# Optimization experiments

Measured on AMD Instinct MI355X. Metric: run time of the kernel, lower is better.

## Reference

```python
import jax, jax.numpy as jnp
import numpy as np

NU, B, N, D = 3, 16, 1024, 256  # n_utils, batch, tokens per util, embed dim


def l2norm(x, axis=-1, eps=1e-12):
    # F.normalize over channel dim: x / max(||x||_2, eps)
    n = jnp.linalg.norm(x, axis=axis, keepdims=True)
    return x / jnp.maximum(n, eps)


def setup_inputs() -> dict:
    key = jax.random.key(0)
    ks = jax.random.split(key, 20)
    s = 0.05
    return {
        "u0": jax.random.normal(ks[0], (B, N, D), jnp.float32),
        "u1": jax.random.normal(ks[1], (B, N, D), jnp.float32),
        "u2": jax.random.normal(ks[2], (B, N, D), jnp.float32),
        # Unary per util: embed Conv1d(D,D,1), feature_reduce Conv1d(D,1,1)
        "Wu": jax.random.normal(ks[3], (NU, D, D), jnp.float32) * s,
        "bu": jax.random.normal(ks[4], (NU, D), jnp.float32) * s,
        "wr": jax.random.normal(ks[5], (NU, D), jnp.float32) * s,
        "br": jax.random.normal(ks[6], (NU,), jnp.float32) * s,
        # Self Pairwise per util: embed_X, embed_Y Conv1d(D,D,1)
        "Wsx": jax.random.normal(ks[7], (NU, D, D), jnp.float32) * s,
        "bsx": jax.random.normal(ks[8], (NU, D), jnp.float32) * s,
        "Wsy": jax.random.normal(ks[9], (NU, D, D), jnp.float32) * s,
        "bsy": jax.random.normal(ks[10], (NU, D), jnp.float32) * s,
        # Cross Pairwise per ordered pair (i,j), i!=j (diagonal unused)
        "Wpx": jax.random.normal(ks[11], (NU, NU, D, D), jnp.float32) * s,
        "bpx": jax.random.normal(ks[12], (NU, NU, D), jnp.float32) * s,
        "Wpy": jax.random.normal(ks[13], (NU, NU, D, D), jnp.float32) * s,
        "bpy": jax.random.normal(ks[14], (NU, NU, D), jnp.float32) * s,
        # reduce_potentials: (i,i) -> Conv1d(4,1,1,bias=False); (i,j) -> Conv1d(3,1,1,bias=False)
        "wdiag": jax.random.normal(ks[15], (NU, 4), jnp.float32) * s,
        "wpair": jax.random.normal(ks[16], (NU, NU, 3), jnp.float32) * s,
    }


def _forward(u0, u1, u2, Wu, bu, wr, br, Wsx, bsx, Wsy, bsy,
             Wpx, bpx, Wpy, bpy, wdiag, wpair):
    U = jnp.stack([u0, u1, u2])  # (NU, b, n, d)

    # --- Unary potentials (eval mode: dropout = identity) ---
    Xe = jnp.einsum('ubnd,ued->ubne', U, Wu) + bu[:, None, None, :]
    unary = jnp.einsum('ubne,ue->ubn', jax.nn.relu(Xe), wr) + br[:, None, None]  # (NU,b,n)

    # --- Self Pairwise (x_spatial_dim=None path): embed, cosine-normalize over channels, affinity, mean ---
    Xs = l2norm(jnp.einsum('ubnd,ued->ubne', U, Wsx) + bsx[:, None, None, :])
    Ys = l2norm(jnp.einsum('ubnd,ued->ubne', U, Wsy) + bsy[:, None, None, :])
    S_self = jnp.einsum('ubne,ubme->ubnm', Xs, Ys)  # (NU,b,n,n)
    self_pot = S_self.mean(axis=3)                   # X_poten only (Y is None)  (NU,b,n)

    # --- Cross Pairwise over all ordered pairs (u,v) ---
    Xp = l2norm(jnp.einsum('ubnd,uved->uvbne', U, Wpx) + bpx[:, :, None, None, :])
    Yp = l2norm(jnp.einsum('vbnd,uved->uvbne', U, Wpy) + bpy[:, :, None, None, :])
    S = jnp.einsum('uvbne,uvbme->uvbnm', Xp, Yp)     # (NU,NU,b,n,n)
    pot_x = S.mean(axis=4)  # poten for util u in pair (u,v): (NU,NU,b,n)
    pot_y = S.mean(axis=3)  # poten for util v in pair (u,v): (NU,NU,b,n)

    # --- Reduce potentials per (target i, source j), softmax-attend over source tokens ---
    rows = []
    for i in range(NU):
        row = []
        for j in range(NU):
            if i == j:
                pots = [unary[i], self_pot[i]] + [pot_x[i, k] for k in range(NU) if k != i]
                w = wdiag[i]            # (4,)
            else:
                pots = [unary[j], self_pot[j], pot_y[i, j]]
                w = wpair[i, j]         # (3,)
            P = jnp.stack(pots, axis=1)                 # (b, k, n)
            red = jnp.einsum('bkn,k->bn', P, w)         # Conv1d(k,1,1,bias=False)
            a = jax.nn.softmax(red, axis=1)             # (b, n)
            row.append(jnp.einsum('bnd,bn->bd', U[j], a))  # attended feature (b, d)
        rows.append(jnp.stack(row))
    return jnp.stack(rows)  # (NU, NU, b, d)


def reference(u0, u1, u2, Wu, bu, wr, br, Wsx, bsx, Wsy, bsy,
              Wpx, bpx, Wpy, bpy, wdiag, wpair):
    return _forward(u0, u1, u2, Wu, bu, wr, br, Wsx, bsx, Wsy, bsy,
                    Wpx, bpx, Wpy, bpy, wdiag, wpair)
```

## Files before the change

kernel.cpp:

```cpp
#include <hip/hip_runtime.h>
#include <math.h>

#define NU 3
#define BB 16
#define NN 1024
#define DD 256
#define MM (BB*NN)
#define NPAIR 6

#define OFF_UNARY  0
#define OFF_INVXS  (OFF_UNARY + NU*MM)
#define OFF_INVXP  (OFF_INVXS + NU*MM)
#define OFF_INVYP  (OFF_INVXP + NPAIR*MM)
#define OFF_YBAR   (OFF_INVYP + NPAIR*MM)
#define OFF_XPBAR  (OFF_YBAR + NU*BB*DD)
#define OFF_YPBAR  (OFF_XPBAR + NPAIR*BB*DD)
#define OFF_PROJS  (OFF_YPBAR + NPAIR*BB*DD)
#define OFF_PROJX  (OFF_PROJS + NU*BB*DD)
#define OFF_PROJY  (OFF_PROJX + NPAIR*BB*DD)
#define OFF_CSS    (OFF_PROJY + NPAIR*BB*DD)
#define OFF_CSX    (OFF_CSS + NU*BB)
#define OFF_CSY    (OFF_CSX + NPAIR*BB)
#define OFF_SELFP  (OFF_CSY + NPAIR*BB)
#define OFF_POTX   (OFF_SELFP + NU*MM)
#define OFF_POTY   (OFF_POTX + NPAIR*MM)
#define WS_FLOATS  (OFF_POTY + NPAIR*MM)
#define OFF_PROB   (WS_FLOATS + 21*32768)
#define OFF_PART   (OFF_PROB + 9*BB*NN)

typedef _Float16 half8 __attribute__((ext_vector_type(8)));
typedef float f32x4 __attribute__((ext_vector_type(4)));

__device__ __forceinline__ const float* selU(int u, const float* u0, const float* u1, const float* u2) {
    return u == 0 ? u0 : (u == 1 ? u1 : u2);
}
__device__ __forceinline__ half8 cvt8(float4 a, float4 b) {
    half8 h = { (_Float16)a.x,(_Float16)a.y,(_Float16)a.z,(_Float16)a.w,
                (_Float16)b.x,(_Float16)b.y,(_Float16)b.z,(_Float16)b.w };
    return h;
}
__device__ __forceinline__ void gload16(const _Float16* g, _Float16* l) {
    __builtin_amdgcn_global_load_lds(
        (const __attribute__((address_space(1))) void*)g,
        (__attribute__((address_space(3))) void*)l,
        16, 0, 0);
}

__global__ __launch_bounds__(256) void convw_kernel(
    const float* __restrict__ Wu, const float* __restrict__ Wsx, const float* __restrict__ Wsy,
    const float* __restrict__ Wpx, const float* __restrict__ Wpy, float* __restrict__ ws)
{
    const int slot = blockIdx.x;
    const int kc   = blockIdx.y;
    const int tid  = threadIdx.x;
    const int u = slot / 7, s = slot % 7;
    const int j0 = (u==0)?1:0, j1 = (u==2)?1:2;
    const float* W =
        s==0 ? Wu  + (size_t)u*DD*DD :
        s==1 ? Wsx + (size_t)u*DD*DD :
        s==2 ? Wsy + (size_t)u*DD*DD :
        s==3 ? Wpx + (size_t)(u*NU+j0)*DD*DD :
        s==4 ? Wpx + (size_t)(u*NU+j1)*DD*DD :
        s==5 ? Wpy + (size_t)(j0*NU+u)*DD*DD :
               Wpy + (size_t)(j1*NU+u)*DD*DD;
    _Float16* wh = (_Float16*)(ws + WS_FLOATS) + (size_t)slot*65536 + (size_t)kc*8192;
    #pragma unroll
    for (int g = 0; g < 4; ++g) {
        const int idx16 = g*256 + tid;
        const int lane = idx16 & 63;
        const int e  = (idx16 >> 6)*16 + (lane & 15);
        const int k0 = kc*32 + (lane >> 4)*8;
        const float* sp = W + (size_t)e*DD + k0;
        const float4 v0 = *reinterpret_cast<const float4*>(sp);
        const float4 v1 = *reinterpret_cast<const float4*>(sp + 4);
        *reinterpret_cast<half8*>(wh + (size_t)idx16*8) = cvt8(v0, v1);
    }
}

__global__ __launch_bounds__(256, 2) void pass1_kernel(
    const float* __restrict__ u0, const float* __restrict__ u1, const float* __restrict__ u2,
    const float* __restrict__ bu, const float* __restrict__ wr, const float* __restrict__ br,
    const float* __restrict__ bsx, const float* __restrict__ bsy,
    const float* __restrict__ bpx, const float* __restrict__ bpy,
    float* __restrict__ ws)
{
    __shared__ __align__(16) _Float16 Ub[16384];
    __shared__ __align__(16) _Float16 Wb[2][8192];
    __shared__ float ep_sum[4][64];
    __shared__ float ep_inv[64];

    const int tid  = threadIdx.x;
    const int u    = blockIdx.y;
    const int row0 = blockIdx.x * 64;
    const int b    = row0 >> 10;

    const int j0 = (u==0)?1:0, j1 = (u==2)?1:2;
    const int px0 = u*2, px1 = u*2+1;
    const int py0 = (u==0)?2:((u==1)?0:1);
    const int py1 = (u==0)?4:((u==1)?5:3);

    const float* src = selU(u,u0,u1,u2);
    const _Float16* whU = (const _Float16*)(ws + WS_FLOATS) + (size_t)u*7*65536;

    const int lane = tid & 63, wq = tid >> 6;
    const int l15 = lane & 15, lg = lane >> 4;
    const int swz = (l15 >> 1) & 3;
    const int kxor = (lg ^ swz) * 8;

    f32x4 acc[4][4];
    #pragma unroll
    for (int m = 0; m < 4; ++m)
        #pragma unroll
        for (int n = 0; n < 4; ++n) acc[m][n] = (f32x4)0.f;

#define STAGE(T, BUF) { \
    const _Float16* gsb = whU + (size_t)((T) >> 3)*65536 + (size_t)((T) & 7)*8192 \
                        + (size_t)(wq*4)*512 + (size_t)lane*8; \
    _Pragma("unroll") \
    for (int i_ = 0; i_ < 4; ++i_) \
        gload16(gsb + i_*512, &Wb[BUF][(wq*4 + i_)*512]); }

    STAGE(0, 0)

    #pragma unroll
    for (int c = 0; c < 8; ++c) {
        const int G2 = c*256 + tid;
        const int t  = G2 >> 5;
        const int gk = G2 & 31;
        const int kc = gk >> 2, kg = gk & 3;
        const float* p = src + (size_t)(row0 + t)*DD + gk*8;
        const float4 v0 = *reinterpret_cast<const float4*>(p);
        const float4 v1 = *reinterpret_cast<const float4*>(p + 4);
        const int kgs = kg ^ ((t >> 1) & 3);
        *reinterpret_cast<half8*>(&Ub[kc*2048 + t*32 + kgs*8]) = cvt8(v0, v1);
    }
    __syncthreads();

    for (int s = 0; s < 7; ++s) {
        #pragma unroll
        for (int kc = 0; kc < 8; ++kc) {
            const int t = s*8 + kc;
            const int cur = t & 1;
            if (t < 55) STAGE(t+1, cur^1)
            half8 af0 = *reinterpret_cast<const half8*>(&Ub[kc*2048 + (     l15)*32 + kxor]);
            half8 af1 = *reinterpret_cast<const half8*>(&Ub[kc*2048 + (16 + l15)*32 + kxor]);
            half8 af2 = *reinterpret_cast<const half8*>(&Ub[kc*2048 + (32 + l15)*32 + kxor]);
            half8 af3 = *reinterpret_cast<const half8*>(&Ub[kc*2048 + (48 + l15)*32 + kxor]);
            #pragma unroll
            for (int n = 0; n < 4; ++n) {
                const half8 bf = *reinterpret_cast<const half8*>(&Wb[cur][(wq*4 + n)*512 + lane*8]);
                acc[0][n] = __builtin_amdgcn_mfma_f32_16x16x32_f16(af0, bf, acc[0][n],0,0,0);
                acc[1][n] = __builtin_amdgcn_mfma_f32_16x16x32_f16(af1, bf, acc[1][n],0,0,0);
                acc[2][n] = __builtin_amdgcn_mfma_f32_16x16x32_f16(af2, bf, acc[2][n],0,0,0);
                acc[3][n] = __builtin_amdgcn_mfma_f32_16x16x32_f16(af3, bf, acc[3][n],0,0,0);
            }
            __syncthreads();
        }

        const float* bias =
            s==0 ? bu  + u*DD :
            s==1 ? bsx + u*DD :
            s==2 ? bsy + u*DD :
            s==3 ? bpx + (u*NU+j0)*DD :
            s==4 ? bpx + (u*NU+j1)*DD :
            s==5 ? bpy + (j0*NU+u)*DD :
                   bpy + (j1*NU+u)*DD;
        float bv[4];
        #pragma unroll
        for (int n = 0; n < 4; ++n) bv[n] = bias[wq*64 + n*16 + l15];
        #pragma unroll
        for (int m = 0; m < 4; ++m)
            #pragma unroll
            for (int n = 0; n < 4; ++n)
                #pragma unroll
                for (int r = 0; r < 4; ++r) acc[m][n][r] += bv[n];

        if (s == 0) {
            float wrv[4];
            #pragma unroll
            for (int n = 0; n < 4; ++n) wrv[n] = wr[u*DD + wq*64 + n*16 + l15];
            float pm[4][4];
            #pragma unroll
            for (int m = 0; m < 4; ++m)
                #pragma unroll
                for (int r = 0; r < 4; ++r) {
                    float t = 0.f;
                    #pragma unroll
                    for (int n = 0; n < 4; ++n) t = fmaf(fmaxf(acc[m][n][r], 0.f), wrv[n], t);
                    pm[m][r] = t;
                }
            #pragma unroll
            for (int mask = 1; mask <= 8; mask <<= 1)
                #pragma unroll
                for (int m = 0; m < 4; ++m)
                    #pragma unroll
                    for (int r = 0; r < 4; ++r) pm[m][r] += __shfl_xor(pm[m][r], mask);
            if (l15 == 0) {
                #pragma unroll
                for (int m = 0; m < 4; ++m)
                    #pragma unroll
                    for (int r = 0; r < 4; ++r) ep_sum[wq][m*16 + lg*4 + r] = pm[m][r];
            }
            __syncthreads();
            if (tid < 64)
                ws[OFF_UNARY + (size_t)u*MM + row0 + tid] =
                    ep_sum[0][tid]+ep_sum[1][tid]+ep_sum[2][tid]+ep_sum[3][tid] + br[u];
        } else {
            float pm[4][4];
            #pragma unroll
            for (int m = 0; m < 4; ++m)
                #pragma unroll
                for (int r = 0; r < 4; ++r) {
                    float t = 0.f;
                    #pragma unroll
                    for (int n = 0; n < 4; ++n) t = fmaf(acc[m][n][r], acc[m][n][r], t);
                    pm[m][r] = t;
                }
            #pragma unroll
            for (int mask = 1; mask <= 8; mask <<= 1)
                #pragma unroll
                for (int m = 0; m < 4; ++m)
                    #pragma unroll
                    for (int r = 0; r < 4; ++r) pm[m][r] += __shfl_xor(pm[m][r], mask);
            if (l15 == 0) {
                #pragma unroll
                for (int m = 0; m < 4; ++m)
                    #pragma unroll
                    for (int r = 0; r < 4; ++r) ep_sum[wq][m*16 + lg*4 + r] = pm[m][r];
            }
            __syncthreads();
            if (tid < 64) {
                const float ssum = ep_sum[0][tid]+ep_sum[1][tid]+ep_sum[2][tid]+ep_sum[3][tid];
                const float inv = 1.f / fmaxf(sqrtf(ssum), 1e-12f);
                ep_inv[tid] = inv;
                if (s == 1)      ws[OFF_INVXS + (size_t)u  *MM + row0 + tid] = inv;
                else if (s == 3) ws[OFF_INVXP + (size_t)px0*MM + row0 + tid] = inv;
                else if (s == 4) ws[OFF_INVXP + (size_t)px1*MM + row0 + tid] = inv;
                else if (s == 5) ws[OFF_INVYP + (size_t)py0*MM + row0 + tid] = inv;
                else if (s == 6) ws[OFF_INVYP + (size_t)py1*MM + row0 + tid] = inv;
            }
            __syncthreads();
            if (s >= 2) {
                float invv[4][4];
                #pragma unroll
                for (int m = 0; m < 4; ++m)
                    #pragma unroll
                    for (int r = 0; r < 4; ++r) invv[m][r] = ep_inv[m*16 + lg*4 + r];
                float qn[4];
                #pragma unroll
                for (int n = 0; n < 4; ++n) {
                    float t = 0.f;
                    #pragma unroll
                    for (int m = 0; m < 4; ++m)
                        #pragma unroll
                        for (int r = 0; r < 4; ++r) t = fmaf(acc[m][n][r], invv[m][r], t);
                    qn[n] = t;
                }
                #pragma unroll
                for (int n = 0; n < 4; ++n) {
                    qn[n] += __shfl_xor(qn[n], 16);
                    qn[n] += __shfl_xor(qn[n], 32);
                }
                float* bar =
                    s==2 ? ws + OFF_YBAR  + ((size_t)u  *BB + b)*DD :
                    s==3 ? ws + OFF_XPBAR + ((size_t)px0*BB + b)*DD :
                    s==4 ? ws + OFF_XPBAR + ((size_t)px1*BB + b)*DD :
                    s==5 ? ws + OFF_YPBAR + ((size_t)py0*BB + b)*DD :
                           ws + OFF_YPBAR + ((size_t)py1*BB + b)*DD;
                if (lane < 16) {
                    #pragma unroll
                    for (int n = 0; n < 4; ++n)
                        atomicAdd(&bar[wq*64 + n*16 + lane], qn[n]);
                }
            }
        }
        #pragma unroll
        for (int m = 0; m < 4; ++m)
            #pragma unroll
            for (int n = 0; n < 4; ++n) acc[m][n] = (f32x4)0.f;
        __syncthreads();
    }
#undef STAGE
}

__global__ __launch_bounds__(256) void proj_kernel(
    const float* __restrict__ Wsx, const float* __restrict__ bsx,
    const float* __restrict__ Wpx, const float* __restrict__ bpx,
    const float* __restrict__ Wpy, const float* __restrict__ bpy,
    float* __restrict__ ws)
{
    __shared__ float barl[DD];
    __shared__ float redl[256];
    const int task = blockIdx.x >> 4;
    const int b    = blockIdx.x & 15;
    const int tid  = threadIdx.x;
    const float *W, *bias, *barp;
    float *projp, *csp;
    if (task < 3) {
        const int uu = task;
        W = Wsx + (size_t)uu*DD*DD; bias = bsx + uu*DD;
        barp  = ws + OFF_YBAR  + ((size_t)uu*BB + b)*DD;
        projp = ws + OFF_PROJS + ((size_t)uu*BB + b)*DD;
        csp   = ws + OFF_CSS + uu*BB + b;
    } else if (task < 9) {
        const int p = task - 3; const int i = p>>1;
        const int j = (p&1) == 0 ? (i==0?1:0) : (i==2?1:2);
        W = Wpx + (size_t)(i*NU+j)*DD*DD; bias = bpx + (i*NU+j)*DD;
        barp  = ws + OFF_YPBAR + ((size_t)p*BB + b)*DD;
        projp = ws + OFF_PROJX + ((size_t)p*BB + b)*DD;
        csp   = ws + OFF_CSX + p*BB + b;
    } else {
        const int p = task - 9; const int i = p>>1;
        const int j = (p&1) == 0 ? (i==0?1:0) : (i==2?1:2);
        W = Wpy + (size_t)(i*NU+j)*DD*DD; bias = bpy + (i*NU+j)*DD;
        barp  = ws + OFF_XPBAR + ((size_t)p*BB + b)*DD;
        projp = ws + OFF_PROJY + ((size_t)p*BB + b)*DD;
        csp   = ws + OFF_CSY + p*BB + b;
    }
    barl[tid] = barp[tid] * (1.f / NN);
    __syncthreads();
    float s = 0.f;
    for (int e = 0; e < DD; ++e) s = fmaf(W[(size_t)e*DD + tid], barl[e], s);
    projp[tid] = s;
    redl[tid] = bias[tid] * barl[tid];
    __syncthreads();
    for (int st = 128; st > 0; st >>= 1) {
        if (tid < st) redl[tid] += redl[tid + st];
        __syncthreads();
    }
    if (tid == 0) *csp = redl[0];
}

__global__ __launch_bounds__(256) void pots_kernel(
    const float* __restrict__ u0, const float* __restrict__ u1, const float* __restrict__ u2,
    float* __restrict__ ws)
{
    __shared__ float projl[5][DD];
    __shared__ float csl[5];
    const int u    = blockIdx.y;
    const int row0 = blockIdx.x * 32;
    const int b    = row0 >> 10;
    const int tid  = threadIdx.x;
    const int px0 = u*2, px1 = u*2+1;
    const int py0 = (u==0)?2:((u==1)?0:1);
    const int py1 = (u==0)?4:((u==1)?5:3);

    projl[0][tid] = ws[OFF_PROJS + ((size_t)u  *BB + b)*DD + tid];
    projl[1][tid] = ws[OFF_PROJX + ((size_t)px0*BB + b)*DD + tid];
    projl[2][tid] = ws[OFF_PROJX + ((size_t)px1*BB + b)*DD + tid];
    projl[3][tid] = ws[OFF_PROJY + ((size_t)py0*BB + b)*DD + tid];
    projl[4][tid] = ws[OFF_PROJY + ((size_t)py1*BB + b)*DD + tid];
    if (tid == 0) {
        csl[0] = ws[OFF_CSS + u*BB + b];
        csl[1] = ws[OFF_CSX + px0*BB + b];
        csl[2] = ws[OFF_CSX + px1*BB + b];
        csl[3] = ws[OFF_CSY + py0*BB + b];
        csl[4] = ws[OFF_CSY + py1*BB + b];
    }
    __syncthreads();
    const float* src = selU(u,u0,u1,u2);
    const int token = tid >> 3, q = tid & 7;
    const int row = row0 + token;
    float a0=0.f,a1=0.f,a2=0.f,a3=0.f,a4=0.f;
    #pragma unroll
    for (int cc = 0; cc < 8; ++cc) {
        const int d0 = q*32 + cc*4;
        const float4 v  = *reinterpret_cast<const float4*>(src + (size_t)row*DD + d0);
        const float4 p0 = *reinterpret_cast<const float4*>(&projl[0][d0]);
        const float4 p1 = *reinterpret_cast<const float4*>(&projl[1][d0]);
        const float4 p2 = *reinterpret_cast<const float4*>(&projl[2][d0]);
        const float4 p3 = *reinterpret_cast<const float4*>(&projl[3][d0]);
        const float4 p4 = *reinterpret_cast<const float4*>(&projl[4][d0]);
        a0 = fmaf(v.x,p0.x,fmaf(v.y,p0.y,fmaf(v.z,p0.z,fmaf(v.w,p0.w,a0))));
        a1 = fmaf(v.x,p1.x,fmaf(v.y,p1.y,fmaf(v.z,p1.z,fmaf(v.w,p1.w,a1))));
        a2 = fmaf(v.x,p2.x,fmaf(v.y,p2.y,fmaf(v.z,p2.z,fmaf(v.w,p2.w,a2))));
        a3 = fmaf(v.x,p3.x,fmaf(v.y,p3.y,fmaf(v.z,p3.z,fmaf(v.w,p3.w,a3))));
        a4 = fmaf(v.x,p4.x,fmaf(v.y,p4.y,fmaf(v.z,p4.z,fmaf(v.w,p4.w,a4))));
    }
    #pragma unroll
    for (int mask = 1; mask <= 4; mask <<= 1) {
        a0 += __shfl_xor(a0, mask, 8);
        a1 += __shfl_xor(a1, mask, 8);
        a2 += __shfl_xor(a2, mask, 8);
        a3 += __shfl_xor(a3, mask, 8);
        a4 += __shfl_xor(a4, mask, 8);
    }
    if (q == 0) {
        ws[OFF_SELFP + (size_t)u  *MM + row] = (a0 + csl[0]) * ws[OFF_INVXS + (size_t)u  *MM + row];
        ws[OFF_POTX  + (size_t)px0*MM + row] = (a1 + csl[1]) * ws[OFF_INVXP + (size_t)px0*MM + row];
        ws[OFF_POTX  + (size_t)px1*MM + row] = (a2 + csl[2]) * ws[OFF_INVXP + (size_t)px1*MM + row];
        ws[OFF_POTY  + (size_t)py0*MM + row] = (a3 + csl[3]) * ws[OFF_INVYP + (size_t)py0*MM + row];
        ws[OFF_POTY  + (size_t)py1*MM + row] = (a4 + csl[4]) * ws[OFF_INVYP + (size_t)py1*MM + row];
    }
}

__global__ __launch_bounds__(256) void attend_logits_kernel(
    const float* __restrict__ wdiag, const float* __restrict__ wpair,
    float* __restrict__ ws)
{
    __shared__ float el[3][NN];
    __shared__ float redl[256];
    const int c = blockIdx.x;
    const int j = c >> 4, b = c & 15;
    const int tid = threadIdx.x;

    #pragma unroll
    for (int i = 0; i < 3; ++i) {
        if (i == j) {
            const int p1 = i*2, p2 = i*2+1;
            const float w0 = wdiag[i*4+0], w1 = wdiag[i*4+1], w2 = wdiag[i*4+2], w3 = wdiag[i*4+3];
            for (int n = tid; n < NN; n += 256) {
                const int row = b*NN + n;
                el[i][n] = w0*ws[OFF_UNARY + i*MM + row] + w1*ws[OFF_SELFP + i*MM + row]
                         + w2*ws[OFF_POTX + p1*MM + row] + w3*ws[OFF_POTX + p2*MM + row];
            }
        } else {
            const int p = i*2 + (j > i ? j-1 : j);
            const float w0 = wpair[(i*3+j)*3+0], w1 = wpair[(i*3+j)*3+1], w2 = wpair[(i*3+j)*3+2];
            for (int n = tid; n < NN; n += 256) {
                const int row = b*NN + n;
                el[i][n] = w0*ws[OFF_UNARY + j*MM + row] + w1*ws[OFF_SELFP + j*MM + row]
                         + w2*ws[OFF_POTY + p*MM + row];
            }
        }
    }
    __syncthreads();
    #pragma unroll
    for (int i = 0; i < 3; ++i) {
        float m = -1e30f;
        for (int n = tid; n < NN; n += 256) m = fmaxf(m, el[i][n]);
        redl[tid] = m; __syncthreads();
        for (int st = 128; st > 0; st >>= 1) {
            if (tid < st) redl[tid] = fmaxf(redl[tid], redl[tid+st]);
            __syncthreads();
        }
        m = redl[0];
        __syncthreads();
        float ss = 0.f;
        for (int n = tid; n < NN; n += 256) {
            const float e = expf(el[i][n] - m);
            el[i][n] = e;
            ss += e;
        }
        redl[tid] = ss; __syncthreads();
        for (int st = 128; st > 0; st >>= 1) {
            if (tid < st) redl[tid] += redl[tid+st];
            __syncthreads();
        }
        const float invS = 1.f / redl[0];
        __syncthreads();
        for (int n = tid; n < NN; n += 256)
            ws[OFF_PROB + ((size_t)(i*3+j)*BB + b)*NN + n] = el[i][n] * invS;
    }
}

__global__ __launch_bounds__(256) void attend_sum_kernel(
    const float* __restrict__ u0, const float* __restrict__ u1, const float* __restrict__ u2,
    const float* __restrict__ ws, float* __restrict__ wso)
{
    __shared__ float pl[3][128];
    const int x  = blockIdx.x;
    const int jb = x >> 3, ch = x & 7;
    const int j = jb >> 4, b = jb & 15;
    const int tid = threadIdx.x;

    for (int t = tid; t < 384; t += 256) {
        const int i = t >> 7, n = t & 127;
        pl[i][n] = ws[OFF_PROB + ((size_t)(i*3+j)*BB + b)*NN + ch*128 + n];
    }
    __syncthreads();
    const float* Uj = selU(j, u0, u1, u2) + ((size_t)b*NN + ch*128)*DD;
    float a0 = 0.f, a1 = 0.f, a2 = 0.f;
    #pragma unroll 4
    for (int n = 0; n < 128; ++n) {
        const float v = Uj[(size_t)n*DD + tid];
        a0 = fmaf(pl[0][n], v, a0);
        a1 = fmaf(pl[1][n], v, a1);
        a2 = fmaf(pl[2][n], v, a2);
    }
    wso[OFF_PART + (((size_t)(0*3+j)*BB + b)*8 + ch)*DD + tid] = a0;
    wso[OFF_PART + (((size_t)(1*3+j)*BB + b)*8 + ch)*DD + tid] = a1;
    wso[OFF_PART + (((size_t)(2*3+j)*BB + b)*8 + ch)*DD + tid] = a2;
}

__global__ __launch_bounds__(256) void attend_reduce_kernel(
    const float* __restrict__ ws, float* __restrict__ out)
{
    const int ijb = blockIdx.x;
    const int tid = threadIdx.x;
    float s = 0.f;
    #pragma unroll
    for (int ch = 0; ch < 8; ++ch)
        s += ws[OFF_PART + ((size_t)ijb*8 + ch)*DD + tid];
    out[(size_t)ijb*DD + tid] = s;
}

extern "C" void kernel_launch(void* const* d_in, const int* in_sizes, int n_in,
                              void* d_out, int out_size, void* d_ws, size_t ws_size,
                              hipStream_t stream)
{
    (void)in_sizes; (void)n_in; (void)out_size; (void)ws_size;
    const float* u0    = (const float*)d_in[0];
    const float* u1    = (const float*)d_in[1];
    const float* u2    = (const float*)d_in[2];
    const float* Wu    = (const float*)d_in[3];
    const float* bu    = (const float*)d_in[4];
    const float* wr    = (const float*)d_in[5];
    const float* br    = (const float*)d_in[6];
    const float* Wsx   = (const float*)d_in[7];
    const float* bsx   = (const float*)d_in[8];
    const float* Wsy   = (const float*)d_in[9];
    const float* bsy   = (const float*)d_in[10];
    const float* Wpx   = (const float*)d_in[11];
    const float* bpx   = (const float*)d_in[12];
    const float* Wpy   = (const float*)d_in[13];
    const float* bpy   = (const float*)d_in[14];
    const float* wdiag = (const float*)d_in[15];
    const float* wpair = (const float*)d_in[16];
    float* ws  = (float*)d_ws;
    float* out = (float*)d_out;

    hipMemsetAsync(ws + OFF_YBAR, 0, (size_t)(NU + 2*NPAIR)*BB*DD*sizeof(float), stream);

    dim3 gw(21, 8);
    convw_kernel<<<gw, 256, 0, stream>>>(Wu, Wsx, Wsy, Wpx, Wpy, ws);

    dim3 g1(MM/64, 3);
    pass1_kernel<<<g1, 256, 0, stream>>>(u0,u1,u2,bu,wr,br,bsx,bsy,bpx,bpy,ws);

    proj_kernel<<<15*BB, 256, 0, stream>>>(Wsx,bsx,Wpx,bpx,Wpy,bpy,ws);
    dim3 g2(MM/32, 3);
    pots_kernel<<<g2, 256, 0, stream>>>(u0,u1,u2,ws);

    attend_logits_kernel<<<3*BB, 256, 0, stream>>>(wdiag, wpair, ws);
    attend_sum_kernel<<<3*BB*8, 256, 0, stream>>>(u0,u1,u2, ws, ws);
    attend_reduce_kernel<<<9*BB, 256, 0, stream>>>(ws, out);
}
```

Baseline: 154.5 us.

## Hold activations in registers and pipeline weights through per-wave LDS ring

The weight fp16 layout is reordered so each wave loads its own contiguous fragment slab. Pass1 now keeps all A fragments (64 rows x 256 k) in registers, read once from LDS. Weights stream through a private 4-deep LDS ring per wave, using explicit vmcnt waits instead of a block-wide __syncthreads every k-chunk. Blocks also rotate which of the 7 weight slots they start with, to spread load over L2/HBM. This removes block barriers from the inner loop and deepens prefetch, at the cost of many more VGPRs (af alone is 128 registers), which risks spills or lower occupancy under launch_bounds(256,2).

```diff
diff --git a/kernel.cpp b/kernel.cpp
--- a/kernel.cpp
+++ b/kernel.cpp
@@ -63,17 +63,18 @@
         s==4 ? Wpx + (size_t)(u*NU+j1)*DD*DD :
         s==5 ? Wpy + (size_t)(j0*NU+u)*DD*DD :
                Wpy + (size_t)(j1*NU+u)*DD*DD;
-    _Float16* wh = (_Float16*)(ws + WS_FLOATS) + (size_t)slot*65536 + (size_t)kc*8192;
+    _Float16* wh = (_Float16*)(ws + WS_FLOATS) + (size_t)slot*65536;
     #pragma unroll
     for (int g = 0; g < 4; ++g) {
         const int idx16 = g*256 + tid;
+        const int et   = idx16 >> 6;
         const int lane = idx16 & 63;
-        const int e  = (idx16 >> 6)*16 + (lane & 15);
+        const int e  = et*16 + (lane & 15);
         const int k0 = kc*32 + (lane >> 4)*8;
         const float* sp = W + (size_t)e*DD + k0;
         const float4 v0 = *reinterpret_cast<const float4*>(sp);
         const float4 v1 = *reinterpret_cast<const float4*>(sp + 4);
-        *reinterpret_cast<half8*>(wh + (size_t)idx16*8) = cvt8(v0, v1);
+        *reinterpret_cast<half8*>(wh + ((size_t)(et*8 + kc)*64 + lane)*8) = cvt8(v0, v1);
     }
 }
 
@@ -84,8 +85,7 @@
     const float* __restrict__ bpx, const float* __restrict__ bpy,
     float* __restrict__ ws)
 {
-    __shared__ __align__(16) _Float16 Ub[16384];
-    __shared__ __align__(16) _Float16 Wb[2][8192];
+    __shared__ __align__(16) _Float16 pool[32768];
     __shared__ float ep_sum[4][64];
     __shared__ float ep_inv[64];
 
@@ -107,20 +107,46 @@
     const int swz = (l15 >> 1) & 3;
     const int kxor = (lg ^ swz) * 8;
 
+    const _Float16* wfrag = whU + (size_t)wq*16384 + (size_t)lane*8;
+    _Float16* ringw = &pool[wq*8192];
+
+    const int rot = blockIdx.x % 7;
+
     f32x4 acc[4][4];
     #pragma unroll
     for (int m = 0; m < 4; ++m)
         #pragma unroll
         for (int n = 0; n < 4; ++n) acc[m][n] = (f32x4)0.f;
 
-#define STAGE(T, BUF) { \
-    const _Float16* gsb = whU + (size_t)((T) >> 3)*65536 + (size_t)((T) & 7)*8192 \
-                        + (size_t)(wq*4)*512 + (size_t)lane*8; \
+    half8 af[4][8];
+
+#define STAGE(T) { \
+    const int sg_ = (((T) >> 3) + rot) % 7; \
+    const int kcg_ = (T) & 7; \
+    const _Float16* g_ = wfrag + (size_t)sg_*65536 + (size_t)kcg_*512; \
+    _Float16* l_ = ringw + ((T) & 3)*2048; \
     _Pragma("unroll") \
-    for (int i_ = 0; i_ < 4; ++i_) \
-        gload16(gsb + i_*512, &Wb[BUF][(wq*4 + i_)*512]); }
-
-    STAGE(0, 0)
+    for (int n_ = 0; n_ < 4; ++n_) \
+        gload16(g_ + (size_t)n_*4096, l_ + n_*512); }
+
+#define SLABC(BASE, KCI) { \
+    const _Float16* rb_ = ringw + (((BASE) + (KCI)) & 3)*2048 + lane*8; \
+    const half8 bf0_ = *reinterpret_cast<const half8*>(rb_); \
+    const half8 bf1_ = *reinterpret_cast<const half8*>(rb_ + 512); \
+    const half8 bf2_ = *reinterpret_cast<const half8*>(rb_ + 1024); \
+    const half8 bf3_ = *reinterpret_cast<const half8*>(rb_ + 1536); \
+    _Pragma("unroll") \
+    for (int m_ = 0; m_ < 4; ++m_) { \
+        acc[m_][0] = __builtin_amdgcn_mfma_f32_16x16x32_f16(af[m_][KCI], bf0_, acc[m_][0],0,0,0); \
+        acc[m_][1] = __builtin_amdgcn_mfma_f32_16x16x32_f16(af[m_][KCI], bf1_, acc[m_][1],0,0,0); \
+        acc[m_][2] = __builtin_amdgcn_mfma_f32_16x16x32_f16(af[m_][KCI], bf2_, acc[m_][2],0,0,0); \
+        acc[m_][3] = __builtin_amdgcn_mfma_f32_16x16x32_f16(af[m_][KCI], bf3_, acc[m_][3],0,0,0); \
+    } }
+
+#define WAITV(NLIT) { \
+    __builtin_amdgcn_sched_barrier(0); \
+    asm volatile("s_waitcnt vmcnt(" NLIT ")" ::: "memory"); \
+    __builtin_amdgcn_sched_barrier(0); }
 
     #pragma unroll
     for (int c = 0; c < 8; ++c) {
@@ -132,29 +158,47 @@
         const float4 v0 = *reinterpret_cast<const float4*>(p);
         const float4 v1 = *reinterpret_cast<const float4*>(p + 4);
         const int kgs = kg ^ ((t >> 1) & 3);
-        *reinterpret_cast<half8*>(&Ub[kc*2048 + t*32 + kgs*8]) = cvt8(v0, v1);
-    }
-    __syncthreads();
-
-    for (int s = 0; s < 7; ++s) {
+        *reinterpret_cast<half8*>(&pool[kc*2048 + t*32 + kgs*8]) = cvt8(v0, v1);
+    }
+    __syncthreads();
+
+    #pragma unroll
+    for (int kc = 0; kc < 8; ++kc)
         #pragma unroll
-        for (int kc = 0; kc < 8; ++kc) {
-            const int t = s*8 + kc;
-            const int cur = t & 1;
-            if (t < 55) STAGE(t+1, cur^1)
-            half8 af0 = *reinterpret_cast<const half8*>(&Ub[kc*2048 + (     l15)*32 + kxor]);
-            half8 af1 = *reinterpret_cast<const half8*>(&Ub[kc*2048 + (16 + l15)*32 + kxor]);
-            half8 af2 = *reinterpret_cast<const half8*>(&Ub[kc*2048 + (32 + l15)*32 + kxor]);
-            half8 af3 = *reinterpret_cast<const half8*>(&Ub[kc*2048 + (48 + l15)*32 + kxor]);
-            #pragma unroll
-            for (int n = 0; n < 4; ++n) {
-                const half8 bf = *reinterpret_cast<const half8*>(&Wb[cur][(wq*4 + n)*512 + lane*8]);
-                acc[0][n] = __builtin_amdgcn_mfma_f32_16x16x32_f16(af0, bf, acc[0][n],0,0,0);
-                acc[1][n] = __builtin_amdgcn_mfma_f32_16x16x32_f16(af1, bf, acc[1][n],0,0,0);
-                acc[2][n] = __builtin_amdgcn_mfma_f32_16x16x32_f16(af2, bf, acc[2][n],0,0,0);
-                acc[3][n] = __builtin_amdgcn_mfma_f32_16x16x32_f16(af3, bf, acc[3][n],0,0,0);
-            }
-            __syncthreads();
+        for (int m = 0; m < 4; ++m)
+            af[m][kc] = *reinterpret_cast<const half8*>(&pool[kc*2048 + (m*16 + l15)*32 + kxor]);
+    __syncthreads();
+
+    STAGE(0)
+    STAGE(1)
+    STAGE(2)
+
+    for (int si = 0; si < 7; ++si) {
+        const int base = si*8;
+        const int s = (si + rot) % 7;
+
+        if (si < 6) {
+            #pragma unroll
+            for (int kci = 0; kci < 8; ++kci) {
+                STAGE(base + kci + 3)
+                WAITV("12")
+                SLABC(base, kci)
+            }
+        } else {
+            #pragma unroll
+            for (int kci = 0; kci < 8; ++kci) {
+                if (kci < 5) {
+                    STAGE(base + kci + 3)
+                    WAITV("12")
+                } else if (kci == 5) {
+                    WAITV("8")
+                } else if (kci == 6) {
+                    WAITV("4")
+                } else {
+                    WAITV("0")
+                }
+                SLABC(base, kci)
+            }
         }
 
         const float* bias =
@@ -281,6 +325,8 @@
         __syncthreads();
     }
 #undef STAGE
+#undef SLABC
+#undef WAITV
 }
 
 __global__ __launch_bounds__(256) void proj_kernel(
```

Result: slower. 164.4 us (+6.4%).
